# Kernel tuning notes

Hardware: AMD Instinct MI355X
Metric: run time of the kernel (lower is better)

## Reference

```python
import jax, jax.numpy as jnp
import numpy as np

SEQ_LEN = 2048
EMB = 512
BATCH = 8


def _xavier_uniform(key, shape):
    fan_in, fan_out = shape[0], shape[1]
    bound = float(np.sqrt(6.0 / (fan_in + fan_out)))
    return jax.random.uniform(key, shape, dtype=jnp.float32, minval=-bound, maxval=bound)


def setup_inputs() -> dict:
    key = jax.random.key(0)
    kx, k1, k2 = jax.random.split(key, 3)
    x = jax.random.normal(kx, (BATCH, EMB, SEQ_LEN), dtype=jnp.float32)
    weight1 = _xavier_uniform(k1, (EMB, EMB))
    weight2 = _xavier_uniform(k2, (EMB, EMB))
    return {"x": x, "weight1": weight1, "weight2": weight2}


def reference(x, weight1, weight2):
    # x: [b, e, s]
    s = x.shape[-1]
    # projections: O(b*s*e^2)
    fitnesses1 = jnp.einsum('bes,ef->bfs', x, weight1)   # [b, e, s]
    fitnesses2 = jnp.einsum('bfs,ef->bes', x, weight2)   # [b, e, s]
    # s x t interaction matrix: O(b*s^2*e)
    weight = jnp.einsum('bes,bet->bst', fitnesses1, fitnesses2)  # [b, s, t]
    # zero strictly-upper triangle (t > s), as in torch.triu(..., diagonal=1)
    mask = jnp.triu(jnp.ones((s, s), dtype=bool), k=1)
    weight = jnp.where(mask, jnp.zeros((), dtype=weight.dtype), weight)
    fitnesses = jnp.einsum('bst,bet->bes', weight, x)    # [b, e, s]
    avg_fitness = jnp.einsum('bes,bes->be', x, fitnesses)[..., None]  # [b, e, 1]
    net_fitnesses = fitnesses - avg_fitness
    x_next = x + x * net_fitnesses
    return jax.nn.relu(x_next)
```

## Files before the change

### kernel.cpp

```cpp
#include <hip/hip_runtime.h>
#include <hip/hip_bf16.h>
#include <stdint.h>


#define SEQ 2048
#define EMB 512
#define NBATCH 8

typedef unsigned short u16;
typedef __bf16 bf16x8 __attribute__((ext_vector_type(8)));
typedef float f32x4 __attribute__((ext_vector_type(4)));
typedef u16 u16x8 __attribute__((ext_vector_type(8)));

#define AS1 __attribute__((address_space(1)))
#define AS3 __attribute__((address_space(3)))

#define SBAR do { __builtin_amdgcn_sched_barrier(0); __builtin_amdgcn_s_barrier(); \
                  __builtin_amdgcn_sched_barrier(0); } while (0)
#define LGKM0 do { asm volatile("s_waitcnt lgkmcnt(0)" ::: "memory"); \
                   __builtin_amdgcn_sched_barrier(0); } while (0)

__device__ __forceinline__ u16 f2bf(float f) {
  uint32_t u = __builtin_bit_cast(uint32_t, f);
  uint32_t r = u + 0x7FFFu + ((u >> 16) & 1u);
  return (u16)(r >> 16);
}
__device__ __forceinline__ float bf2f(u16 u) {
  return __builtin_bit_cast(float, (uint32_t)u << 16);
}
__device__ __forceinline__ void gld_lds16(const void* g, void* l) {
  __builtin_amdgcn_global_load_lds((AS1 uint32_t*)g, (AS3 uint32_t*)l, 16, 0, 0);
}

__global__ __launch_bounds__(256) void prep_x_kernel(const float* __restrict__ x,
    u16* __restrict__ xb, u16* __restrict__ xbT) {
  __shared__ float tile[64][65];
  const int b = blockIdx.z;
  const int s0 = blockIdx.x * 64, e0 = blockIdx.y * 64;
  const float* xin = x + (size_t)b * EMB * SEQ;
  const int tid = threadIdx.x;
  #pragma unroll
  for (int it = 0; it < 4; ++it) {
    int idx = it * 256 + tid;
    int r = idx >> 4, c4 = idx & 15;
    float4 v = *(const float4*)(xin + (size_t)(e0 + r) * SEQ + s0 + c4 * 4);
    tile[r][c4 * 4 + 0] = v.x; tile[r][c4 * 4 + 1] = v.y;
    tile[r][c4 * 4 + 2] = v.z; tile[r][c4 * 4 + 3] = v.w;
  }
  __syncthreads();
  u16* ob = xb + (size_t)b * EMB * SEQ;
  #pragma unroll
  for (int it = 0; it < 2; ++it) {
    int idx = it * 256 + tid; int r = idx >> 3, c8 = idx & 7;
    u16x8 o;
    #pragma unroll
    for (int q = 0; q < 8; ++q) o[q] = f2bf(tile[r][c8 * 8 + q]);
    *(u16x8*)(ob + (size_t)(e0 + r) * SEQ + s0 + c8 * 8) = o;
  }
  u16* obT = xbT + (size_t)b * SEQ * EMB;
  #pragma unroll
  for (int it = 0; it < 2; ++it) {
    int idx = it * 256 + tid; int r = idx >> 3, c8 = idx & 7;
    u16x8 o;
    #pragma unroll
    for (int q = 0; q < 8; ++q) o[q] = f2bf(tile[c8 * 8 + q][r]);
    *(u16x8*)(obT + (size_t)(s0 + r) * EMB + e0 + c8 * 8) = o;
  }
}

__global__ __launch_bounds__(256) void cast_bf16_kernel(const float* __restrict__ in,
                                                        u16* __restrict__ out, int n4) {
  int i = blockIdx.x * 256 + threadIdx.x;
  if (i >= n4) return;
  float4 v = reinterpret_cast<const float4*>(in)[i];
  ushort4 r;
  r.x = f2bf(v.x); r.y = f2bf(v.y); r.z = f2bf(v.z); r.w = f2bf(v.w);
  reinterpret_cast<ushort4*>(out)[i] = r;
}

__global__ __launch_bounds__(256) void transpose_cast_kernel(const float* __restrict__ in,
    u16* __restrict__ out, int R, int C) {
  __shared__ float tile[32][33];
  const int c0 = blockIdx.x * 32, r0 = blockIdx.y * 32;
  const int tx = threadIdx.x, ty = threadIdx.y;
  #pragma unroll
  for (int i = 0; i < 32; i += 8)
    tile[ty + i][tx] = in[(size_t)(r0 + ty + i) * C + c0 + tx];
  __syncthreads();
  #pragma unroll
  for (int i = 0; i < 32; i += 8)
    out[(size_t)(c0 + ty + i) * R + r0 + tx] = f2bf(tile[tx][ty + i]);
}

struct Smem {
  __align__(16) u16 LA[2][256 * 64];
  __align__(16) u16 LB[2][256 * 64];
};

__device__ __forceinline__ void gemm_pipe(const u16* __restrict__ Ab, int ldA,
    const u16* __restrict__ Bb, int ldB, int nk, Smem& sm, f32x4 (&acc)[8][4]) {
  const int tid  = threadIdx.x;
  const int lane = tid & 63;
  const int wave = tid >> 6;
  const int wr = wave >> 2;
  const int wc = wave & 3;

  auto stage_half = [&](const u16* gbase, int ldG, int rowOff, int kcol, u16* lds) {
    #pragma unroll
    for (int p = 0; p < 2; ++p) {
      int c = p * 512 + tid;
      int row = c >> 3, cc = c & 7;
      int cs = cc ^ (row & 7);
      gld_lds16(gbase + (size_t)(rowOff + row) * ldG + kcol + cs * 8,
                lds + (size_t)(p * 512 + wave * 64) * 8);
    }
  };
  auto ldfrag = [&](const u16* base, int rloc, int c2) -> bf16x8 {
    int cs = c2 ^ (rloc & 7);
    return *reinterpret_cast<const bf16x8*>(base + (size_t)(rloc * 8 + cs) * 8);
  };

  stage_half(Ab, ldA, 0,   0, sm.LA[0]);
  stage_half(Ab, ldA, 128, 0, sm.LA[0] + 8192);
  stage_half(Bb, ldB, 0,   0, sm.LB[0]);
  stage_half(Bb, ldB, 128, 0, sm.LB[0] + 8192);
  if (nk > 1) {
    stage_half(Bb, ldB, 0,   64, sm.LB[1]);
    stage_half(Bb, ldB, 128, 64, sm.LB[1] + 8192);
  }
  if (nk > 1) { asm volatile("s_waitcnt vmcnt(4)" ::: "memory"); }
  else        { asm volatile("s_waitcnt vmcnt(0)" ::: "memory"); }
  SBAR;

  const int ar = lane & 15;
  const int asel = lane >> 4;
  bf16x8 af[4][2], bf0[2][2], bf1[2][2];

  for (int t = 0; t < nk; ++t) {
    const int sel = t & 1;
    const u16* a_ = sm.LA[sel];
    const u16* b_ = sm.LB[sel];

    #pragma unroll
    for (int m = 0; m < 4; ++m)
      #pragma unroll
      for (int kk = 0; kk < 2; ++kk)
        af[m][kk] = ldfrag(a_, wr * 128 + m * 16 + ar, kk * 4 + asel);
    #pragma unroll
    for (int n = 0; n < 2; ++n)
      #pragma unroll
      for (int kk = 0; kk < 2; ++kk)
        bf0[n][kk] = ldfrag(b_, wc * 64 + n * 16 + ar, kk * 4 + asel);
    if (t + 1 < nk) stage_half(Ab, ldA, 0, (t + 1) * 64, sm.LA[sel ^ 1]);
    SBAR; LGKM0;
    __builtin_amdgcn_s_setprio(1);
    #pragma unroll
    for (int m = 0; m < 4; ++m)
      #pragma unroll
      for (int n = 0; n < 2; ++n)
        #pragma unroll
        for (int kk = 0; kk < 2; ++kk)
          acc[m][n] = __builtin_amdgcn_mfma_f32_16x16x32_bf16(af[m][kk], bf0[n][kk], acc[m][n], 0, 0, 0);
    __builtin_amdgcn_s_setprio(0);
    SBAR;

    #pragma unroll
    for (int n = 0; n < 2; ++n)
      #pragma unroll
      for (int kk = 0; kk < 2; ++kk)
        bf1[n][kk] = ldfrag(b_, wc * 64 + (n + 2) * 16 + ar, kk * 4 + asel);
    if (t + 1 < nk) stage_half(Ab, ldA, 128, (t + 1) * 64, sm.LA[sel ^ 1] + 8192);
    SBAR; LGKM0;
    __builtin_amdgcn_s_setprio(1);
    #pragma unroll
    for (int m = 0; m < 4; ++m)
      #pragma unroll
      for (int n = 0; n < 2; ++n)
        #pragma unroll
        for (int kk = 0; kk < 2; ++kk)
          acc[m][n + 2] = __builtin_amdgcn_mfma_f32_16x16x32_bf16(af[m][kk], bf1[n][kk], acc[m][n + 2], 0, 0, 0);
    __builtin_amdgcn_s_setprio(0);
    SBAR;

    #pragma unroll
    for (int m = 0; m < 4; ++m)
      #pragma unroll
      for (int kk = 0; kk < 2; ++kk)
        af[m][kk] = ldfrag(a_, wr * 128 + 64 + m * 16 + ar, kk * 4 + asel);
    if (t + 2 < nk) stage_half(Bb, ldB, 0, (t + 2) * 64, sm.LB[sel]);
    SBAR; LGKM0;
    __builtin_amdgcn_s_setprio(1);
    #pragma unroll
    for (int m = 0; m < 4; ++m)
      #pragma unroll
      for (int n = 0; n < 2; ++n)
        #pragma unroll
        for (int kk = 0; kk < 2; ++kk)
          acc[m + 4][n + 2] = __builtin_amdgcn_mfma_f32_16x16x32_bf16(af[m][kk], bf1[n][kk], acc[m + 4][n + 2], 0, 0, 0);
    __builtin_amdgcn_s_setprio(0);
    SBAR;

    if (t + 2 < nk) stage_half(Bb, ldB, 128, (t + 2) * 64, sm.LB[sel] + 8192);
    SBAR;
    __builtin_amdgcn_s_setprio(1);
    #pragma unroll
    for (int m = 0; m < 4; ++m)
      #pragma unroll
      for (int n = 0; n < 2; ++n)
        #pragma unroll
        for (int kk = 0; kk < 2; ++kk)
          acc[m + 4][n] = __builtin_amdgcn_mfma_f32_16x16x32_bf16(af[m][kk], bf0[n][kk], acc[m + 4][n], 0, 0, 0);
    __builtin_amdgcn_s_setprio(0);
    if (t + 1 < nk) {
      if (t + 2 < nk) { asm volatile("s_waitcnt vmcnt(4)" ::: "memory"); }
      else            { asm volatile("s_waitcnt vmcnt(0)" ::: "memory"); }
    }
    SBAR;
  }
}

template<int MODE>
__global__ __launch_bounds__(512, 2) void k_gemm(
    const u16* __restrict__ X1, const u16* __restrict__ X2,
    const u16* __restrict__ X3, const u16* __restrict__ X4,
    u16* __restrict__ O16, u16* __restrict__ O16b, float* __restrict__ O32) {
  __shared__ Smem sm;
  const int tid  = threadIdx.x;
  const int lane = tid & 63;
  const int wave = tid >> 6;
  const int wr = wave >> 2;
  const int wc = wave & 3;
  const int bz = blockIdx.z;

  f32x4 acc[8][4];
  #pragma unroll
  for (int i = 0; i < 8; ++i)
    #pragma unroll
    for (int j = 0; j < 4; ++j) acc[i][j] = (f32x4){0.f, 0.f, 0.f, 0.f};

  const int r0 = (lane >> 4) * 4;
  const int cn = lane & 15;

  if (MODE == 0) {
    const int bm = blockIdx.x, bn = blockIdx.y;
    const u16* A = X1 + (size_t)bz * SEQ * EMB + (size_t)(bm * 256) * 512;
    const u16* B = X2 + (size_t)(bn * 256) * 512;
    gemm_pipe(A, 512, B, 512, 8, sm, acc);
    u16* C = O16 + (size_t)bz * SEQ * 1024;
    #pragma unroll
    for (int m = 0; m < 8; ++m)
      #pragma unroll
      for (int n = 0; n < 4; ++n)
        #pragma unroll
        for (int r = 0; r < 4; ++r) {
          int lr = wr * 128 + m * 16 + r0 + r, lc = wc * 64 + n * 16 + cn;
          C[(size_t)(bm * 256 + lr) * 1024 + bn * 256 + lc] = f2bf(acc[m][n][r]);
        }
  } else if (MODE == 1) {
    const int xx = blockIdx.x;
    if (xx < 16) {
      const int m2 = xx >> 3, n2 = xx & 7;
      const u16* A = X1 + (size_t)(m2 * 256) * 512;
      const u16* B = X2 + (size_t)bz * SEQ * EMB + (size_t)(n2 * 256) * 512;
      gemm_pipe(A, 512, B, 512, 8, sm, acc);
      u16* C = O16 + (size_t)bz * EMB * SEQ;
      #pragma unroll
      for (int m = 0; m < 8; ++m)
        #pragma unroll
        for (int n = 0; n < 4; ++n)
          #pragma unroll
          for (int r = 0; r < 4; ++r) {
            int lr = wr * 128 + m * 16 + r0 + r, lc = wc * 64 + n * 16 + cn;
            C[(size_t)(m2 * 256 + lr) * SEQ + n2 * 256 + lc] = f2bf(acc[m][n][r]);
          }
    } else {
      const int i = xx - 16;
      const u16* Fb = X3 + (size_t)bz * SEQ * 1024;
      const u16* A = Fb + (size_t)(i * 256) * 1024;
      const u16* B = Fb + 512 + (size_t)(i * 256) * 1024;
      gemm_pipe(A, 1024, B, 1024, 8, sm, acc);
      u16* C = O16b + (size_t)(bz * 8 + i) * 256 * 256;
      #pragma unroll
      for (int m = 0; m < 8; ++m)
        #pragma unroll
        for (int n = 0; n < 4; ++n)
          #pragma unroll
          for (int r = 0; r < 4; ++r) {
            int lr = wr * 128 + m * 16 + r0 + r, lc = wc * 64 + n * 16 + cn;
            float v = (lc > lr) ? 0.f : acc[m][n][r];
            C[(size_t)lr * 256 + lc] = f2bf(v);
          }
    }
  } else if (MODE == 2) {
    const int m = blockIdx.x >> 1, n = blockIdx.x & 1;
    const int b = bz >> 3, j = bz & 7;
    const u16* A = X1 + (size_t)b * EMB * SEQ + (size_t)(m * 256) * SEQ + j * 256;
    const u16* B = X2 + (size_t)b * EMB * SEQ + (size_t)(n * 256) * SEQ + j * 256;
    gemm_pipe(A, SEQ, B, SEQ, 4, sm, acc);
    u16* C = O16 + (size_t)(b * 8 + j) * EMB * EMB;
    #pragma unroll
    for (int mm = 0; mm < 8; ++mm)
      #pragma unroll
      for (int nn = 0; nn < 4; ++nn)
        #pragma unroll
        for (int r = 0; r < 4; ++r) {
          int lr = wr * 128 + mm * 16 + r0 + r, lc = wc * 64 + nn * 16 + cn;
          C[(size_t)(m * 256 + lr) * EMB + n * 256 + lc] = f2bf(acc[mm][nn][r]);
        }
  } else {
    const int m = blockIdx.x & 1, i = blockIdx.x >> 1;
    if (i > 0) {
      const u16* A = X1 + (size_t)(bz * 7 + i - 1) * EMB * EMB + (size_t)(m * 256) * 512;
      const u16* B = X2 + (size_t)bz * SEQ * 1024 + (size_t)(i * 256) * 1024;
      gemm_pipe(A, 512, B, 1024, 8, sm, acc);
    }
    {
      const u16* A = X3 + (size_t)bz * EMB * SEQ + (size_t)(m * 256) * SEQ + i * 256;
      const u16* B = X4 + (size_t)(bz * 8 + i) * 256 * 256;
      gemm_pipe(A, SEQ, B, 256, 4, sm, acc);
    }
    float* C = O32 + (size_t)bz * EMB * SEQ;
    #pragma unroll
    for (int mm = 0; mm < 8; ++mm)
      #pragma unroll
      for (int nn = 0; nn < 4; ++nn)
        #pragma unroll
        for (int r = 0; r < 4; ++r) {
          int lr = wr * 128 + mm * 16 + r0 + r, lc = wc * 64 + nn * 16 + cn;
          C[(size_t)(m * 256 + lr) * SEQ + i * 256 + lc] = acc[mm][nn][r];
        }
  }
}

__global__ __launch_bounds__(256) void k_prefix(const u16* __restrict__ Gc,
                                                u16* __restrict__ Gp) {
  const int b = blockIdx.z;
  const size_t base = ((size_t)blockIdx.x * 256 + threadIdx.x) * 8;
  float run[8] = {0.f, 0.f, 0.f, 0.f, 0.f, 0.f, 0.f, 0.f};
  #pragma unroll
  for (int j = 0; j < 7; ++j) {
    u16x8 v = *(const u16x8*)(Gc + (size_t)(b * 8 + j) * EMB * EMB + base);
    u16x8 o;
    #pragma unroll
    for (int q = 0; q < 8; ++q) { run[q] += bf2f(v[q]); o[q] = f2bf(run[q]); }
    *(u16x8*)(Gp + (size_t)(b * 7 + j) * EMB * EMB + base) = o;
  }
}

__global__ __launch_bounds__(256) void finalize_kernel(const u16* __restrict__ xb,
    const float* __restrict__ fit, float* __restrict__ out) {
  const size_t row = blockIdx.x;
  const u16* xr = xb + row * SEQ;
  const float* fr = fit + row * SEQ;
  float* orow = out + row * SEQ;
  const int tid = threadIdx.x;

  float xv[2][4]; float4 fv[2];
  float part = 0.f;
  #pragma unroll
  for (int i = 0; i < 2; ++i) {
    const int s0 = i * 1024 + tid * 4;
    ushort4 xu = *reinterpret_cast<const ushort4*>(xr + s0);
    xv[i][0] = bf2f(xu.x); xv[i][1] = bf2f(xu.y); xv[i][2] = bf2f(xu.z); xv[i][3] = bf2f(xu.w);
    fv[i] = reinterpret_cast<const float4*>(fr)[i * 256 + tid];
    part += xv[i][0] * fv[i].x + xv[i][1] * fv[i].y + xv[i][2] * fv[i].z + xv[i][3] * fv[i].w;
  }
  #pragma unroll
  for (int off = 1; off < 64; off <<= 1) part += __shfl_xor(part, off);
  __shared__ float wsum[4];
  const int wave = tid >> 6, lane = tid & 63;
  if (lane == 0) wsum[wave] = part;
  __syncthreads();
  const float avg = wsum[0] + wsum[1] + wsum[2] + wsum[3];

  #pragma unroll
  for (int i = 0; i < 2; ++i) {
    float4 o;
    o.x = xv[i][0] * (1.f + fv[i].x - avg); o.x = o.x > 0.f ? o.x : 0.f;
    o.y = xv[i][1] * (1.f + fv[i].y - avg); o.y = o.y > 0.f ? o.y : 0.f;
    o.z = xv[i][2] * (1.f + fv[i].z - avg); o.z = o.z > 0.f ? o.z : 0.f;
    o.w = xv[i][3] * (1.f + fv[i].w - avg); o.w = o.w > 0.f ? o.w : 0.f;
    reinterpret_cast<float4*>(orow)[i * 256 + tid] = o;
  }
}

extern "C" void kernel_launch(void* const* d_in, const int* in_sizes, int n_in,
                              void* d_out, int out_size, void* d_ws, size_t ws_size,
                              hipStream_t stream) {
  const float* x  = (const float*)d_in[0];
  const float* W1 = (const float*)d_in[1];
  const float* W2 = (const float*)d_in[2];
  float* out = (float*)d_out;

  char* ws = (char*)d_ws;
  const size_t nX = (size_t)NBATCH * EMB * SEQ;

  size_t off = 0;
  u16* xb   = (u16*)(ws + off); off += nX * 2;
  u16* Fcat = (u16*)(ws + off); off += (size_t)NBATCH * SEQ * 1024 * 2;
  const size_t offOverlay = off;
  u16* xbT  = (u16*)(ws + off); off += nX * 2;
  u16* Wcat = (u16*)(ws + off); off += (size_t)1024 * 512 * 2;
  u16* F2n  = (u16*)(ws + off); off += nX * 2;
  u16* Sd   = (u16*)(ws + off); off += (size_t)NBATCH * 8 * 256 * 256 * 2;
  u16* Gc   = (u16*)(ws + off); off += (size_t)NBATCH * 8 * EMB * EMB * 2;
  u16* Gp   = (u16*)(ws + off); off += (size_t)NBATCH * 7 * EMB * EMB * 2;
  float* fit = (float*)(ws + offOverlay);

  prep_x_kernel<<<dim3(SEQ / 64, EMB / 64, NBATCH), 256, 0, stream>>>(x, xb, xbT);
  transpose_cast_kernel<<<dim3(EMB / 32, EMB / 32), dim3(32, 8), 0, stream>>>(W1, Wcat, EMB, EMB);
  cast_bf16_kernel<<<EMB * EMB / 4 / 256, 256, 0, stream>>>(W2, Wcat + (size_t)512 * 512, EMB * EMB / 4);

  k_gemm<0><<<dim3(8, 4, NBATCH), 512, 0, stream>>>(
      xbT, Wcat, nullptr, nullptr, Fcat, nullptr, nullptr);

  k_gemm<1><<<dim3(24, 1, NBATCH), 512, 0, stream>>>(
      Wcat + (size_t)512 * 512, xbT, Fcat, nullptr, F2n, Sd, nullptr);

  k_gemm<2><<<dim3(4, 1, 64), 512, 0, stream>>>(
      xb, F2n, nullptr, nullptr, Gc, nullptr, nullptr);

  k_prefix<<<dim3(128, 1, NBATCH), 256, 0, stream>>>(Gc, Gp);

  k_gemm<3><<<dim3(16, 1, NBATCH), 512, 0, stream>>>(
      Gp, Fcat, xb, Sd, nullptr, nullptr, fit);

  finalize_kernel<<<NBATCH * EMB, 256, 0, stream>>>(xb, fit, out);
}
```

Baseline: 133.7 us.

## Shrink GEMM tiles to 128x128 with 256 threads and drop double-buffered pipeline

Replaces the 256x256, 8-wave, double-buffered GEMM pipeline with a simple single-buffered 128x128 tile on 4 waves, and quadruples the grid of every GEMM launch. More blocks fill the GPU better and allow three resident blocks per CU. The sub-blocks that are entirely above the diagonal in the masked S tile only write zeros instead of running a matmul. The cost is that global loads are no longer overlapped with MFMA work, there is less reuse per tile, and each K step adds a full wait and barrier.

Result: slower. 140.2 us (+4.8%).

```diff
diff --git a/kernel.cpp b/kernel.cpp
--- a/kernel.cpp
+++ b/kernel.cpp
@@ -92,27 +92,24 @@
     out[(size_t)(c0 + ty + i) * R + r0 + tx] = f2bf(tile[tx][ty + i]);
 }
 
-struct Smem {
-  __align__(16) u16 LA[2][256 * 64];
-  __align__(16) u16 LB[2][256 * 64];
+struct Smem128 {
+  __align__(16) u16 LA[128 * 64];
+  __align__(16) u16 LB[128 * 64];
 };
 
-__device__ __forceinline__ void gemm_pipe(const u16* __restrict__ Ab, int ldA,
-    const u16* __restrict__ Bb, int ldB, int nk, Smem& sm, f32x4 (&acc)[8][4]) {
-  const int tid  = threadIdx.x;
-  const int lane = tid & 63;
-  const int wave = tid >> 6;
-  const int wr = wave >> 2;
-  const int wc = wave & 3;
-
-  auto stage_half = [&](const u16* gbase, int ldG, int rowOff, int kcol, u16* lds) {
-    #pragma unroll
-    for (int p = 0; p < 2; ++p) {
-      int c = p * 512 + tid;
-      int row = c >> 3, cc = c & 7;
-      int cs = cc ^ (row & 7);
-      gld_lds16(gbase + (size_t)(rowOff + row) * ldG + kcol + cs * 8,
-                lds + (size_t)(p * 512 + wave * 64) * 8);
+__device__ __forceinline__ void gemm128(const u16* __restrict__ Ab, int ldA,
+    const u16* __restrict__ Bb, int ldB, int nk, Smem128& sm, f32x4 (&acc)[4][4]) {
+  const int tid = threadIdx.x, lane = tid & 63, wave = tid >> 6;
+  const int wr = wave >> 1, wc = wave & 1;
+  const int ar = lane & 15, asel = lane >> 4;
+
+  auto stage = [&](const u16* g, int ld, int kcol, u16* lds) {
+    #pragma unroll
+    for (int it = 0; it < 4; ++it) {
+      int L = it * 256 + tid;
+      int row = L >> 3, cc = L & 7, cs = cc ^ (row & 7);
+      gld_lds16(g + (size_t)row * ld + kcol + cs * 8,
+                lds + (size_t)(it * 256 + wave * 64) * 8);
     }
   };
   auto ldfrag = [&](const u16* base, int rloc, int c2) -> bf16x8 {
@@ -120,121 +117,52 @@
     return *reinterpret_cast<const bf16x8*>(base + (size_t)(rloc * 8 + cs) * 8);
   };
 
-  stage_half(Ab, ldA, 0,   0, sm.LA[0]);
-  stage_half(Ab, ldA, 128, 0, sm.LA[0] + 8192);
-  stage_half(Bb, ldB, 0,   0, sm.LB[0]);
-  stage_half(Bb, ldB, 128, 0, sm.LB[0] + 8192);
-  if (nk > 1) {
-    stage_half(Bb, ldB, 0,   64, sm.LB[1]);
-    stage_half(Bb, ldB, 128, 64, sm.LB[1] + 8192);
-  }
-  if (nk > 1) { asm volatile("s_waitcnt vmcnt(4)" ::: "memory"); }
-  else        { asm volatile("s_waitcnt vmcnt(0)" ::: "memory"); }
-  SBAR;
-
-  const int ar = lane & 15;
-  const int asel = lane >> 4;
-  bf16x8 af[4][2], bf0[2][2], bf1[2][2];
-
   for (int t = 0; t < nk; ++t) {
-    const int sel = t & 1;
-    const u16* a_ = sm.LA[sel];
-    const u16* b_ = sm.LB[sel];
-
+    stage(Ab, ldA, t * 64, sm.LA);
+    stage(Bb, ldB, t * 64, sm.LB);
+    asm volatile("s_waitcnt vmcnt(0)" ::: "memory");
+    SBAR;
+    bf16x8 af[4][2], bf[4][2];
     #pragma unroll
     for (int m = 0; m < 4; ++m)
       #pragma unroll
       for (int kk = 0; kk < 2; ++kk)
-        af[m][kk] = ldfrag(a_, wr * 128 + m * 16 + ar, kk * 4 + asel);
-    #pragma unroll
-    for (int n = 0; n < 2; ++n)
+        af[m][kk] = ldfrag(sm.LA, wr * 64 + m * 16 + ar, kk * 4 + asel);
+    #pragma unroll
+    for (int n = 0; n < 4; ++n)
       #pragma unroll
       for (int kk = 0; kk < 2; ++kk)
-        bf0[n][kk] = ldfrag(b_, wc * 64 + n * 16 + ar, kk * 4 + asel);
-    if (t + 1 < nk) stage_half(Ab, ldA, 0, (t + 1) * 64, sm.LA[sel ^ 1]);
-    SBAR; LGKM0;
+        bf[n][kk] = ldfrag(sm.LB, wc * 64 + n * 16 + ar, kk * 4 + asel);
+    LGKM0;
     __builtin_amdgcn_s_setprio(1);
     #pragma unroll
     for (int m = 0; m < 4; ++m)
       #pragma unroll
-      for (int n = 0; n < 2; ++n)
+      for (int n = 0; n < 4; ++n)
         #pragma unroll
         for (int kk = 0; kk < 2; ++kk)
-          acc[m][n] = __builtin_amdgcn_mfma_f32_16x16x32_bf16(af[m][kk], bf0[n][kk], acc[m][n], 0, 0, 0);
+          acc[m][n] = __builtin_amdgcn_mfma_f32_16x16x32_bf16(af[m][kk], bf[n][kk], acc[m][n], 0, 0, 0);
     __builtin_amdgcn_s_setprio(0);
     SBAR;
-
-    #pragma unroll
-    for (int n = 0; n < 2; ++n)
-      #pragma unroll
-      for (int kk = 0; kk < 2; ++kk)
-        bf1[n][kk] = ldfrag(b_, wc * 64 + (n + 2) * 16 + ar, kk * 4 + asel);
-    if (t + 1 < nk) stage_half(Ab, ldA, 128, (t + 1) * 64, sm.LA[sel ^ 1] + 8192);
-    SBAR; LGKM0;
-    __builtin_amdgcn_s_setprio(1);
-    #pragma unroll
-    for (int m = 0; m < 4; ++m)
-      #pragma unroll
-      for (int n = 0; n < 2; ++n)
-        #pragma unroll
-        for (int kk = 0; kk < 2; ++kk)
-          acc[m][n + 2] = __builtin_amdgcn_mfma_f32_16x16x32_bf16(af[m][kk], bf1[n][kk], acc[m][n + 2], 0, 0, 0);
-    __builtin_amdgcn_s_setprio(0);
-    SBAR;
-
-    #pragma unroll
-    for (int m = 0; m < 4; ++m)
-      #pragma unroll
-      for (int kk = 0; kk < 2; ++kk)
-        af[m][kk] = ldfrag(a_, wr * 128 + 64 + m * 16 + ar, kk * 4 + asel);
-    if (t + 2 < nk) stage_half(Bb, ldB, 0, (t + 2) * 64, sm.LB[sel]);
-    SBAR; LGKM0;
-    __builtin_amdgcn_s_setprio(1);
-    #pragma unroll
-    for (int m = 0; m < 4; ++m)
-      #pragma unroll
-      for (int n = 0; n < 2; ++n)
-        #pragma unroll
-        for (int kk = 0; kk < 2; ++kk)
-          acc[m + 4][n + 2] = __builtin_amdgcn_mfma_f32_16x16x32_bf16(af[m][kk], bf1[n][kk], acc[m + 4][n + 2], 0, 0, 0);
-    __builtin_amdgcn_s_setprio(0);
-    SBAR;
-
-    if (t + 2 < nk) stage_half(Bb, ldB, 128, (t + 2) * 64, sm.LB[sel] + 8192);
-    SBAR;
-    __builtin_amdgcn_s_setprio(1);
-    #pragma unroll
-    for (int m = 0; m < 4; ++m)
-      #pragma unroll
-      for (int n = 0; n < 2; ++n)
-        #pragma unroll
-        for (int kk = 0; kk < 2; ++kk)
-          acc[m + 4][n] = __builtin_amdgcn_mfma_f32_16x16x32_bf16(af[m][kk], bf0[n][kk], acc[m + 4][n], 0, 0, 0);
-    __builtin_amdgcn_s_setprio(0);
-    if (t + 1 < nk) {
-      if (t + 2 < nk) { asm volatile("s_waitcnt vmcnt(4)" ::: "memory"); }
-      else            { asm volatile("s_waitcnt vmcnt(0)" ::: "memory"); }
-    }
-    SBAR;
   }
 }
 
 template<int MODE>
-__global__ __launch_bounds__(512, 2) void k_gemm(
+__global__ __launch_bounds__(256, 3) void k_gemm(
     const u16* __restrict__ X1, const u16* __restrict__ X2,
     const u16* __restrict__ X3, const u16* __restrict__ X4,
     u16* __restrict__ O16, u16* __restrict__ O16b, float* __restrict__ O32) {
-  __shared__ Smem sm;
+  __shared__ Smem128 sm;
   const int tid  = threadIdx.x;
   const int lane = tid & 63;
   const int wave = tid >> 6;
-  const int wr = wave >> 2;
-  const int wc = wave & 3;
+  const int wr = wave >> 1;
+  const int wc = wave & 1;
   const int bz = blockIdx.z;
 
-  f32x4 acc[8][4];
-  #pragma unroll
-  for (int i = 0; i < 8; ++i)
+  f32x4 acc[4][4];
+  #pragma unroll
+  for (int i = 0; i < 4; ++i)
     #pragma unroll
     for (int j = 0; j < 4; ++j) acc[i][j] = (f32x4){0.f, 0.f, 0.f, 0.f};
 
@@ -242,92 +170,104 @@
   const int cn = lane & 15;
 
   if (MODE == 0) {
-    const int bm = blockIdx.x, bn = blockIdx.y;
-    const u16* A = X1 + (size_t)bz * SEQ * EMB + (size_t)(bm * 256) * 512;
-    const u16* B = X2 + (size_t)(bn * 256) * 512;
-    gemm_pipe(A, 512, B, 512, 8, sm, acc);
+    const int m = blockIdx.x, n = blockIdx.y;
+    const u16* A = X1 + (size_t)bz * SEQ * EMB + (size_t)(m * 128) * 512;
+    const u16* B = X2 + (size_t)(n * 128) * 512;
+    gemm128(A, 512, B, 512, 8, sm, acc);
     u16* C = O16 + (size_t)bz * SEQ * 1024;
     #pragma unroll
-    for (int m = 0; m < 8; ++m)
-      #pragma unroll
-      for (int n = 0; n < 4; ++n)
+    for (int mm = 0; mm < 4; ++mm)
+      #pragma unroll
+      for (int nn = 0; nn < 4; ++nn)
         #pragma unroll
         for (int r = 0; r < 4; ++r) {
-          int lr = wr * 128 + m * 16 + r0 + r, lc = wc * 64 + n * 16 + cn;
-          C[(size_t)(bm * 256 + lr) * 1024 + bn * 256 + lc] = f2bf(acc[m][n][r]);
+          int lr = wr * 64 + mm * 16 + r0 + r, lc = wc * 64 + nn * 16 + cn;
+          C[(size_t)(m * 128 + lr) * 1024 + n * 128 + lc] = f2bf(acc[mm][nn][r]);
         }
   } else if (MODE == 1) {
     const int xx = blockIdx.x;
-    if (xx < 16) {
-      const int m2 = xx >> 3, n2 = xx & 7;
-      const u16* A = X1 + (size_t)(m2 * 256) * 512;
-      const u16* B = X2 + (size_t)bz * SEQ * EMB + (size_t)(n2 * 256) * 512;
-      gemm_pipe(A, 512, B, 512, 8, sm, acc);
+    if (xx < 64) {
+      const int m2 = xx >> 4, n2 = xx & 15;
+      const u16* A = X1 + (size_t)(m2 * 128) * 512;
+      const u16* B = X2 + (size_t)bz * SEQ * EMB + (size_t)(n2 * 128) * 512;
+      gemm128(A, 512, B, 512, 8, sm, acc);
       u16* C = O16 + (size_t)bz * EMB * SEQ;
       #pragma unroll
-      for (int m = 0; m < 8; ++m)
-        #pragma unroll
-        for (int n = 0; n < 4; ++n)
+      for (int mm = 0; mm < 4; ++mm)
+        #pragma unroll
+        for (int nn = 0; nn < 4; ++nn)
           #pragma unroll
           for (int r = 0; r < 4; ++r) {
-            int lr = wr * 128 + m * 16 + r0 + r, lc = wc * 64 + n * 16 + cn;
-            C[(size_t)(m2 * 256 + lr) * SEQ + n2 * 256 + lc] = f2bf(acc[m][n][r]);
+            int lr = wr * 64 + mm * 16 + r0 + r, lc = wc * 64 + nn * 16 + cn;
+            C[(size_t)(m2 * 128 + lr) * SEQ + n2 * 128 + lc] = f2bf(acc[mm][nn][r]);
           }
     } else {
-      const int i = xx - 16;
+      const int idx = xx - 64;
+      const int i = idx >> 2, p = (idx >> 1) & 1, q = idx & 1;
+      u16* C = O16b + (size_t)(bz * 8 + i) * 256 * 256;
+      if (p == 0 && q == 1) {
+        u16x8 z = {0, 0, 0, 0, 0, 0, 0, 0};
+        #pragma unroll
+        for (int it = 0; it < 8; ++it) {
+          int id2 = it * 256 + tid;
+          int r = id2 >> 4, c8 = id2 & 15;
+          *(u16x8*)(C + (size_t)r * 256 + 128 + c8 * 8) = z;
+        }
+        return;
+      }
       const u16* Fb = X3 + (size_t)bz * SEQ * 1024;
-      const u16* A = Fb + (size_t)(i * 256) * 1024;
-      const u16* B = Fb + 512 + (size_t)(i * 256) * 1024;
-      gemm_pipe(A, 1024, B, 1024, 8, sm, acc);
-      u16* C = O16b + (size_t)(bz * 8 + i) * 256 * 256;
-      #pragma unroll
-      for (int m = 0; m < 8; ++m)
-        #pragma unroll
-        for (int n = 0; n < 4; ++n)
+      const u16* A = Fb + (size_t)(i * 256 + p * 128) * 1024;
+      const u16* B = Fb + 512 + (size_t)(i * 256 + q * 128) * 1024;
+      gemm128(A, 1024, B, 1024, 8, sm, acc);
+      #pragma unroll
+      for (int mm = 0; mm < 4; ++mm)
+        #pragma unroll
+        for (int nn = 0; nn < 4; ++nn)
           #pragma unroll
           for (int r = 0; r < 4; ++r) {
-            int lr = wr * 128 + m * 16 + r0 + r, lc = wc * 64 + n * 16 + cn;
-            float v = (lc > lr) ? 0.f : acc[m][n][r];
-            C[(size_t)lr * 256 + lc] = f2bf(v);
+            int lr = wr * 64 + mm * 16 + r0 + r, lc = wc * 64 + nn * 16 + cn;
+            int grow = p * 128 + lr, gcol = q * 128 + lc;
+            float v = (gcol > grow) ? 0.f : acc[mm][nn][r];
+            C[(size_t)grow * 256 + gcol] = f2bf(v);
           }
     }
   } else if (MODE == 2) {
-    const int m = blockIdx.x >> 1, n = blockIdx.x & 1;
+    const int m = blockIdx.x >> 2, n = blockIdx.x & 3;
     const int b = bz >> 3, j = bz & 7;
-    const u16* A = X1 + (size_t)b * EMB * SEQ + (size_t)(m * 256) * SEQ + j * 256;
-    const u16* B = X2 + (size_t)b * EMB * SEQ + (size_t)(n * 256) * SEQ + j * 256;
-    gemm_pipe(A, SEQ, B, SEQ, 4, sm, acc);
+    const u16* A = X1 + (size_t)b * EMB * SEQ + (size_t)(m * 128) * SEQ + j * 256;
+    const u16* B = X2 + (size_t)b * EMB * SEQ + (size_t)(n * 128) * SEQ + j * 256;
+    gemm128(A, SEQ, B, SEQ, 4, sm, acc);
     u16* C = O16 + (size_t)(b * 8 + j) * EMB * EMB;
     #pragma unroll
-    for (int mm = 0; mm < 8; ++mm)
+    for (int mm = 0; mm < 4; ++mm)
       #pragma unroll
       for (int nn = 0; nn < 4; ++nn)
         #pragma unroll
         for (int r = 0; r < 4; ++r) {
-          int lr = wr * 128 + mm * 16 + r0 + r, lc = wc * 64 + nn * 16 + cn;
-          C[(size_t)(m * 256 + lr) * EMB + n * 256 + lc] = f2bf(acc[mm][nn][r]);
+          int lr = wr * 64 + mm * 16 + r0 + r, lc = wc * 64 + nn * 16 + cn;
+          C[(size_t)(m * 128 + lr) * EMB + n * 128 + lc] = f2bf(acc[mm][nn][r]);
         }
   } else {
-    const int m = blockIdx.x & 1, i = blockIdx.x >> 1;
+    const int m = blockIdx.x >> 1, n = blockIdx.x & 1, i = blockIdx.y;
     if (i > 0) {
-      const u16* A = X1 + (size_t)(bz * 7 + i - 1) * EMB * EMB + (size_t)(m * 256) * 512;
-      const u16* B = X2 + (size_t)bz * SEQ * 1024 + (size_t)(i * 256) * 1024;
-      gemm_pipe(A, 512, B, 1024, 8, sm, acc);
+      const u16* A = X1 + (size_t)(bz * 7 + i - 1) * EMB * EMB + (size_t)(m * 128) * 512;
+      const u16* B = X2 + (size_t)bz * SEQ * 1024 + (size_t)(i * 256 + n * 128) * 1024;
+      gemm128(A, 512, B, 1024, 8, sm, acc);
     }
     {
-      const u16* A = X3 + (size_t)bz * EMB * SEQ + (size_t)(m * 256) * SEQ + i * 256;
-      const u16* B = X4 + (size_t)(bz * 8 + i) * 256 * 256;
-      gemm_pipe(A, SEQ, B, 256, 4, sm, acc);
+      const u16* A = X3 + (size_t)bz * EMB * SEQ + (size_t)(m * 128) * SEQ + i * 256;
+      const u16* B = X4 + (size_t)(bz * 8 + i) * 256 * 256 + (size_t)(n * 128) * 256;
+      gemm128(A, SEQ, B, 256, 4, sm, acc);
     }
     float* C = O32 + (size_t)bz * EMB * SEQ;
     #pragma unroll
-    for (int mm = 0; mm < 8; ++mm)
+    for (int mm = 0; mm < 4; ++mm)
       #pragma unroll
       for (int nn = 0; nn < 4; ++nn)
         #pragma unroll
         for (int r = 0; r < 4; ++r) {
-          int lr = wr * 128 + mm * 16 + r0 + r, lc = wc * 64 + nn * 16 + cn;
-          C[(size_t)(m * 256 + lr) * SEQ + i * 256 + lc] = acc[mm][nn][r];
+          int lr = wr * 64 + mm * 16 + r0 + r, lc = wc * 64 + nn * 16 + cn;
+          C[(size_t)(m * 128 + lr) * SEQ + i * 256 + n * 128 + lc] = acc[mm][nn][r];
         }
   }
 }
@@ -411,18 +351,18 @@
   transpose_cast_kernel<<<dim3(EMB / 32, EMB / 32), dim3(32, 8), 0, stream>>>(W1, Wcat, EMB, EMB);
   cast_bf16_kernel<<<EMB * EMB / 4 / 256, 256, 0, stream>>>(W2, Wcat + (size_t)512 * 512, EMB * EMB / 4);
 
-  k_gemm<0><<<dim3(8, 4, NBATCH), 512, 0, stream>>>(
+  k_gemm<0><<<dim3(16, 8, NBATCH), 256, 0, stream>>>(
       xbT, Wcat, nullptr, nullptr, Fcat, nullptr, nullptr);
 
-  k_gemm<1><<<dim3(24, 1, NBATCH), 512, 0, stream>>>(
+  k_gemm<1><<<dim3(96, 1, NBATCH), 256, 0, stream>>>(
       Wcat + (size_t)512 * 512, xbT, Fcat, nullptr, F2n, Sd, nullptr);
 
-  k_gemm<2><<<dim3(4, 1, 64), 512, 0, stream>>>(
+  k_gemm<2><<<dim3(16, 1, 64), 256, 0, stream>>>(
       xb, F2n, nullptr, nullptr, Gc, nullptr, nullptr);
 
   k_prefix<<<dim3(128, 1, NBATCH), 256, 0, stream>>>(Gc, Gp);
 
-  k_gemm<3><<<dim3(16, 1, NBATCH), 512, 0, stream>>>(
+  k_gemm<3><<<dim3(8, 8, NBATCH), 256, 0, stream>>>(
       Gp, Fcat, xb, Sd, nullptr, nullptr, fit);
 
   finalize_kernel<<<NBATCH * EMB, 256, 0, stream>>>(xb, fit, out);
```

## Merge GEMM launches, fuse weight prep, and chain fitness GEMM phases in one pipeline

Applied to the files above, without the earlier changes.

Merges the two weight-prep kernels into one launch, and moves the F2 projection into the first GEMM launch alongside F1. The Sd diagonal-block GEMM and the per-chunk Gram GEMM now share one launch, so the pipeline has fewer kernel launches and less idle tail per launch. The final GEMM streams both phases (prefix-Gram times F1, then x times masked diagonal) through a single continuous pipeline through a parameter lambda, so there is no pipeline drain between them. It also stores the fitness result in bf16 instead of fp32, which halves that round trip but adds rounding error before the avg reduction.

Result: no change. 135.4 us (+1.3%).

```diff
diff --git a/kernel.cpp b/kernel.cpp
--- a/kernel.cpp
+++ b/kernel.cpp
@@ -68,28 +68,26 @@
   }
 }
 
-__global__ __launch_bounds__(256) void cast_bf16_kernel(const float* __restrict__ in,
-                                                        u16* __restrict__ out, int n4) {
-  int i = blockIdx.x * 256 + threadIdx.x;
-  if (i >= n4) return;
-  float4 v = reinterpret_cast<const float4*>(in)[i];
-  ushort4 r;
-  r.x = f2bf(v.x); r.y = f2bf(v.y); r.z = f2bf(v.z); r.w = f2bf(v.w);
-  reinterpret_cast<ushort4*>(out)[i] = r;
-}
-
-__global__ __launch_bounds__(256) void transpose_cast_kernel(const float* __restrict__ in,
-    u16* __restrict__ out, int R, int C) {
+__global__ __launch_bounds__(256) void prep_w_kernel(const float* __restrict__ W1,
+    const float* __restrict__ W2, u16* __restrict__ Wcat) {
   __shared__ float tile[32][33];
   const int c0 = blockIdx.x * 32, r0 = blockIdx.y * 32;
   const int tx = threadIdx.x, ty = threadIdx.y;
-  #pragma unroll
-  for (int i = 0; i < 32; i += 8)
-    tile[ty + i][tx] = in[(size_t)(r0 + ty + i) * C + c0 + tx];
-  __syncthreads();
-  #pragma unroll
-  for (int i = 0; i < 32; i += 8)
-    out[(size_t)(c0 + ty + i) * R + r0 + tx] = f2bf(tile[tx][ty + i]);
+  if (blockIdx.z == 0) {
+    #pragma unroll
+    for (int i = 0; i < 32; i += 8)
+      tile[ty + i][tx] = W1[(size_t)(r0 + ty + i) * EMB + c0 + tx];
+    __syncthreads();
+    #pragma unroll
+    for (int i = 0; i < 32; i += 8)
+      Wcat[(size_t)(c0 + ty + i) * EMB + r0 + tx] = f2bf(tile[tx][ty + i]);
+  } else {
+    u16* W2b = Wcat + (size_t)512 * 512;
+    #pragma unroll
+    for (int i = 0; i < 32; i += 8)
+      W2b[(size_t)(r0 + ty + i) * EMB + c0 + tx] =
+          f2bf(W2[(size_t)(r0 + ty + i) * EMB + c0 + tx]);
+  }
 }
 
 struct Smem {
@@ -97,21 +95,23 @@
   __align__(16) u16 LB[2][256 * 64];
 };
 
-__device__ __forceinline__ void gemm_pipe(const u16* __restrict__ Ab, int ldA,
-    const u16* __restrict__ Bb, int ldB, int nk, Smem& sm, f32x4 (&acc)[8][4]) {
+template<typename PAR>
+__device__ __forceinline__ void gemm_pipe(PAR par, int nk, Smem& sm, f32x4 (&acc)[8][4]) {
   const int tid  = threadIdx.x;
   const int lane = tid & 63;
   const int wave = tid >> 6;
   const int wr = wave >> 2;
   const int wc = wave & 3;
 
-  auto stage_half = [&](const u16* gbase, int ldG, int rowOff, int kcol, u16* lds) {
+  auto stage_half = [&](int t, int ab, int half, u16* lds) {
+    const u16* g; int ld, k;
+    par(t, ab, g, ld, k);
     #pragma unroll
     for (int p = 0; p < 2; ++p) {
       int c = p * 512 + tid;
       int row = c >> 3, cc = c & 7;
       int cs = cc ^ (row & 7);
-      gld_lds16(gbase + (size_t)(rowOff + row) * ldG + kcol + cs * 8,
+      gld_lds16(g + (size_t)(half * 128 + row) * ld + k + cs * 8,
                 lds + (size_t)(p * 512 + wave * 64) * 8);
     }
   };
@@ -120,13 +120,13 @@
     return *reinterpret_cast<const bf16x8*>(base + (size_t)(rloc * 8 + cs) * 8);
   };
 
-  stage_half(Ab, ldA, 0,   0, sm.LA[0]);
-  stage_half(Ab, ldA, 128, 0, sm.LA[0] + 8192);
-  stage_half(Bb, ldB, 0,   0, sm.LB[0]);
-  stage_half(Bb, ldB, 128, 0, sm.LB[0] + 8192);
+  stage_half(0, 0, 0, sm.LA[0]);
+  stage_half(0, 0, 1, sm.LA[0] + 8192);
+  stage_half(0, 1, 0, sm.LB[0]);
+  stage_half(0, 1, 1, sm.LB[0] + 8192);
   if (nk > 1) {
-    stage_half(Bb, ldB, 0,   64, sm.LB[1]);
-    stage_half(Bb, ldB, 128, 64, sm.LB[1] + 8192);
+    stage_half(1, 1, 0, sm.LB[1]);
+    stage_half(1, 1, 1, sm.LB[1] + 8192);
   }
   if (nk > 1) { asm volatile("s_waitcnt vmcnt(4)" ::: "memory"); }
   else        { asm volatile("s_waitcnt vmcnt(0)" ::: "memory"); }
@@ -151,7 +151,7 @@
       #pragma unroll
       for (int kk = 0; kk < 2; ++kk)
         bf0[n][kk] = ldfrag(b_, wc * 64 + n * 16 + ar, kk * 4 + asel);
-    if (t + 1 < nk) stage_half(Ab, ldA, 0, (t + 1) * 64, sm.LA[sel ^ 1]);
+    if (t + 1 < nk) stage_half(t + 1, 0, 0, sm.LA[sel ^ 1]);
     SBAR; LGKM0;
     __builtin_amdgcn_s_setprio(1);
     #pragma unroll
@@ -169,7 +169,7 @@
       #pragma unroll
       for (int kk = 0; kk < 2; ++kk)
         bf1[n][kk] = ldfrag(b_, wc * 64 + (n + 2) * 16 + ar, kk * 4 + asel);
-    if (t + 1 < nk) stage_half(Ab, ldA, 128, (t + 1) * 64, sm.LA[sel ^ 1] + 8192);
+    if (t + 1 < nk) stage_half(t + 1, 0, 1, sm.LA[sel ^ 1] + 8192);
     SBAR; LGKM0;
     __builtin_amdgcn_s_setprio(1);
     #pragma unroll
@@ -187,7 +187,7 @@
       #pragma unroll
       for (int kk = 0; kk < 2; ++kk)
         af[m][kk] = ldfrag(a_, wr * 128 + 64 + m * 16 + ar, kk * 4 + asel);
-    if (t + 2 < nk) stage_half(Bb, ldB, 0, (t + 2) * 64, sm.LB[sel]);
+    if (t + 2 < nk) stage_half(t + 2, 1, 0, sm.LB[sel]);
     SBAR; LGKM0;
     __builtin_amdgcn_s_setprio(1);
     #pragma unroll
@@ -200,7 +200,7 @@
     __builtin_amdgcn_s_setprio(0);
     SBAR;
 
-    if (t + 2 < nk) stage_half(Bb, ldB, 128, (t + 2) * 64, sm.LB[sel] + 8192);
+    if (t + 2 < nk) stage_half(t + 2, 1, 1, sm.LB[sel] + 8192);
     SBAR;
     __builtin_amdgcn_s_setprio(1);
     #pragma unroll
@@ -223,7 +223,7 @@
 __global__ __launch_bounds__(512, 2) void k_gemm(
     const u16* __restrict__ X1, const u16* __restrict__ X2,
     const u16* __restrict__ X3, const u16* __restrict__ X4,
-    u16* __restrict__ O16, u16* __restrict__ O16b, float* __restrict__ O32) {
+    u16* __restrict__ O16, u16* __restrict__ O16b) {
   __shared__ Smem sm;
   const int tid  = threadIdx.x;
   const int lane = tid & 63;
@@ -242,62 +242,107 @@
   const int cn = lane & 15;
 
   if (MODE == 0) {
-    const int bm = blockIdx.x, bn = blockIdx.y;
-    const u16* A = X1 + (size_t)bz * SEQ * EMB + (size_t)(bm * 256) * 512;
-    const u16* B = X2 + (size_t)(bn * 256) * 512;
-    gemm_pipe(A, 512, B, 512, 8, sm, acc);
-    u16* C = O16 + (size_t)bz * SEQ * 1024;
-    #pragma unroll
-    for (int m = 0; m < 8; ++m)
-      #pragma unroll
-      for (int n = 0; n < 4; ++n)
-        #pragma unroll
-        for (int r = 0; r < 4; ++r) {
-          int lr = wr * 128 + m * 16 + r0 + r, lc = wc * 64 + n * 16 + cn;
-          C[(size_t)(bm * 256 + lr) * 1024 + bn * 256 + lc] = f2bf(acc[m][n][r]);
-        }
+    const int xx = blockIdx.x;
+    const u16* Ap; const u16* Bp;
+    if (xx < 32) {
+      const int m = xx >> 2, n = xx & 3;
+      Ap = X1 + (size_t)bz * SEQ * EMB + (size_t)(m * 256) * 512;
+      Bp = X2 + (size_t)(n * 256) * 512;
+      auto par = [&](int t, int ab, const u16*& g, int& ld, int& k) {
+        g = ab ? Bp : Ap; ld = 512; k = t * 64;
+      };
+      gemm_pipe(par, 8, sm, acc);
+      u16* C = O16 + (size_t)bz * SEQ * 1024;
+      #pragma unroll
+      for (int mm = 0; mm < 8; ++mm)
+        #pragma unroll
+        for (int nn = 0; nn < 4; ++nn)
+          #pragma unroll
+          for (int r = 0; r < 4; ++r) {
+            int lr = wr * 128 + mm * 16 + r0 + r, lc = wc * 64 + nn * 16 + cn;
+            C[(size_t)(m * 256 + lr) * 1024 + n * 256 + lc] = f2bf(acc[mm][nn][r]);
+          }
+    } else {
+      const int m2 = (xx - 32) >> 3, n2 = (xx - 32) & 7;
+      Ap = X2 + (size_t)512 * 512 + (size_t)(m2 * 256) * 512;
+      Bp = X1 + (size_t)bz * SEQ * EMB + (size_t)(n2 * 256) * 512;
+      auto par = [&](int t, int ab, const u16*& g, int& ld, int& k) {
+        g = ab ? Bp : Ap; ld = 512; k = t * 64;
+      };
+      gemm_pipe(par, 8, sm, acc);
+      u16* C = O16b + (size_t)bz * EMB * SEQ;
+      #pragma unroll
+      for (int mm = 0; mm < 8; ++mm)
+        #pragma unroll
+        for (int nn = 0; nn < 4; ++nn)
+          #pragma unroll
+          for (int r = 0; r < 4; ++r) {
+            int lr = wr * 128 + mm * 16 + r0 + r, lc = wc * 64 + nn * 16 + cn;
+            C[(size_t)(m2 * 256 + lr) * SEQ + n2 * 256 + lc] = f2bf(acc[mm][nn][r]);
+          }
+    }
   } else if (MODE == 1) {
     const int xx = blockIdx.x;
-    if (xx < 16) {
-      const int m2 = xx >> 3, n2 = xx & 7;
-      const u16* A = X1 + (size_t)(m2 * 256) * 512;
-      const u16* B = X2 + (size_t)bz * SEQ * EMB + (size_t)(n2 * 256) * 512;
-      gemm_pipe(A, 512, B, 512, 8, sm, acc);
-      u16* C = O16 + (size_t)bz * EMB * SEQ;
-      #pragma unroll
-      for (int m = 0; m < 8; ++m)
-        #pragma unroll
-        for (int n = 0; n < 4; ++n)
+    if (xx < 8) {
+      const int i = xx;
+      const u16* Fb = X1 + (size_t)bz * SEQ * 1024;
+      const u16* Ap = Fb + (size_t)(i * 256) * 1024;
+      const u16* Bp = Fb + 512 + (size_t)(i * 256) * 1024;
+      auto par = [&](int t, int ab, const u16*& g, int& ld, int& k) {
+        g = ab ? Bp : Ap; ld = 1024; k = t * 64;
+      };
+      gemm_pipe(par, 8, sm, acc);
+      u16* C = O16 + (size_t)(bz * 8 + i) * 256 * 256;
+      #pragma unroll
+      for (int mm = 0; mm < 8; ++mm)
+        #pragma unroll
+        for (int nn = 0; nn < 4; ++nn)
           #pragma unroll
           for (int r = 0; r < 4; ++r) {
-            int lr = wr * 128 + m * 16 + r0 + r, lc = wc * 64 + n * 16 + cn;
-            C[(size_t)(m2 * 256 + lr) * SEQ + n2 * 256 + lc] = f2bf(acc[m][n][r]);
+            int lr = wr * 128 + mm * 16 + r0 + r, lc = wc * 64 + nn * 16 + cn;
+            float v = (lc > lr) ? 0.f : acc[mm][nn][r];
+            C[(size_t)lr * 256 + lc] = f2bf(v);
           }
     } else {
-      const int i = xx - 16;
-      const u16* Fb = X3 + (size_t)bz * SEQ * 1024;
-      const u16* A = Fb + (size_t)(i * 256) * 1024;
-      const u16* B = Fb + 512 + (size_t)(i * 256) * 1024;
-      gemm_pipe(A, 1024, B, 1024, 8, sm, acc);
-      u16* C = O16b + (size_t)(bz * 8 + i) * 256 * 256;
-      #pragma unroll
-      for (int m = 0; m < 8; ++m)
-        #pragma unroll
-        for (int n = 0; n < 4; ++n)
+      const int y = xx - 8;
+      const int j = y >> 2, m = (y >> 1) & 1, n = y & 1;
+      const u16* Ap = X2 + (size_t)bz * EMB * SEQ + (size_t)(m * 256) * SEQ + j * 256;
+      const u16* Bp = X3 + (size_t)bz * EMB * SEQ + (size_t)(n * 256) * SEQ + j * 256;
+      auto par = [&](int t, int ab, const u16*& g, int& ld, int& k) {
+        g = ab ? Bp : Ap; ld = SEQ; k = t * 64;
+      };
+      gemm_pipe(par, 4, sm, acc);
+      u16* C = O16b + (size_t)(bz * 8 + j) * EMB * EMB;
+      #pragma unroll
+      for (int mm = 0; mm < 8; ++mm)
+        #pragma unroll
+        for (int nn = 0; nn < 4; ++nn)
           #pragma unroll
           for (int r = 0; r < 4; ++r) {
-            int lr = wr * 128 + m * 16 + r0 + r, lc = wc * 64 + n * 16 + cn;
-            float v = (lc > lr) ? 0.f : acc[m][n][r];
-            C[(size_t)lr * 256 + lc] = f2bf(v);
+            int lr = wr * 128 + mm * 16 + r0 + r, lc = wc * 64 + nn * 16 + cn;
+            C[(size_t)(m * 256 + lr) * EMB + n * 256 + lc] = f2bf(acc[mm][nn][r]);
           }
     }
-  } else if (MODE == 2) {
-    const int m = blockIdx.x >> 1, n = blockIdx.x & 1;
-    const int b = bz >> 3, j = bz & 7;
-    const u16* A = X1 + (size_t)b * EMB * SEQ + (size_t)(m * 256) * SEQ + j * 256;
-    const u16* B = X2 + (size_t)b * EMB * SEQ + (size_t)(n * 256) * SEQ + j * 256;
-    gemm_pipe(A, SEQ, B, SEQ, 4, sm, acc);
-    u16* C = O16 + (size_t)(b * 8 + j) * EMB * EMB;
+  } else {
+    const int i = blockIdx.x >> 1, m = blockIdx.x & 1;
+    const u16* Agp = (i > 0) ? X1 + (size_t)(bz * 7 + i - 1) * EMB * EMB + (size_t)(m * 256) * 512
+                             : X1;
+    const u16* Bf1 = X2 + (size_t)bz * SEQ * 1024 + (size_t)(i * 256) * 1024;
+    const u16* Axb = X3 + (size_t)bz * EMB * SEQ + (size_t)(m * 256) * SEQ;
+    const u16* Bsd = X4 + (size_t)(bz * 8 + i) * 256 * 256;
+    auto par = [&](int t, int ab, const u16*& g, int& ld, int& k) {
+      int tt = (i > 0) ? t : t + 8;
+      if (tt < 8) {
+        if (!ab) { g = Agp; ld = 512;  k = tt * 64; }
+        else     { g = Bf1; ld = 1024; k = tt * 64; }
+      } else {
+        int u = tt - 8;
+        if (!ab) { g = Axb; ld = SEQ; k = i * 256 + u * 64; }
+        else     { g = Bsd; ld = 256; k = u * 64; }
+      }
+    };
+    gemm_pipe(par, (i > 0) ? 12 : 4, sm, acc);
+    u16* C = O16 + (size_t)bz * EMB * SEQ;
     #pragma unroll
     for (int mm = 0; mm < 8; ++mm)
       #pragma unroll
@@ -305,29 +350,7 @@
         #pragma unroll
         for (int r = 0; r < 4; ++r) {
           int lr = wr * 128 + mm * 16 + r0 + r, lc = wc * 64 + nn * 16 + cn;
-          C[(size_t)(m * 256 + lr) * EMB + n * 256 + lc] = f2bf(acc[mm][nn][r]);
-        }
-  } else {
-    const int m = blockIdx.x & 1, i = blockIdx.x >> 1;
-    if (i > 0) {
-      const u16* A = X1 + (size_t)(bz * 7 + i - 1) * EMB * EMB + (size_t)(m * 256) * 512;
-      const u16* B = X2 + (size_t)bz * SEQ * 1024 + (size_t)(i * 256) * 1024;
-      gemm_pipe(A, 512, B, 1024, 8, sm, acc);
-    }
-    {
-      const u16* A = X3 + (size_t)bz * EMB * SEQ + (size_t)(m * 256) * SEQ + i * 256;
-      const u16* B = X4 + (size_t)(bz * 8 + i) * 256 * 256;
-      gemm_pipe(A, SEQ, B, 256, 4, sm, acc);
-    }
-    float* C = O32 + (size_t)bz * EMB * SEQ;
-    #pragma unroll
-    for (int mm = 0; mm < 8; ++mm)
-      #pragma unroll
-      for (int nn = 0; nn < 4; ++nn)
-        #pragma unroll
-        for (int r = 0; r < 4; ++r) {
-          int lr = wr * 128 + mm * 16 + r0 + r, lc = wc * 64 + nn * 16 + cn;
-          C[(size_t)(m * 256 + lr) * SEQ + i * 256 + lc] = acc[mm][nn][r];
+          C[(size_t)(m * 256 + lr) * SEQ + i * 256 + lc] = f2bf(acc[mm][nn][r]);
         }
   }
 }
@@ -348,22 +371,23 @@
 }
 
 __global__ __launch_bounds__(256) void finalize_kernel(const u16* __restrict__ xb,
-    const float* __restrict__ fit, float* __restrict__ out) {
+    const u16* __restrict__ fitb, float* __restrict__ out) {
   const size_t row = blockIdx.x;
   const u16* xr = xb + row * SEQ;
-  const float* fr = fit + row * SEQ;
+  const u16* fr = fitb + row * SEQ;
   float* orow = out + row * SEQ;
   const int tid = threadIdx.x;
 
-  float xv[2][4]; float4 fv[2];
+  float xv[2][4], fv[2][4];
   float part = 0.f;
   #pragma unroll
   for (int i = 0; i < 2; ++i) {
     const int s0 = i * 1024 + tid * 4;
     ushort4 xu = *reinterpret_cast<const ushort4*>(xr + s0);
+    ushort4 fu = *reinterpret_cast<const ushort4*>(fr + s0);
     xv[i][0] = bf2f(xu.x); xv[i][1] = bf2f(xu.y); xv[i][2] = bf2f(xu.z); xv[i][3] = bf2f(xu.w);
-    fv[i] = reinterpret_cast<const float4*>(fr)[i * 256 + tid];
-    part += xv[i][0] * fv[i].x + xv[i][1] * fv[i].y + xv[i][2] * fv[i].z + xv[i][3] * fv[i].w;
+    fv[i][0] = bf2f(fu.x); fv[i][1] = bf2f(fu.y); fv[i][2] = bf2f(fu.z); fv[i][3] = bf2f(fu.w);
+    part += xv[i][0] * fv[i][0] + xv[i][1] * fv[i][1] + xv[i][2] * fv[i][2] + xv[i][3] * fv[i][3];
   }
   #pragma unroll
   for (int off = 1; off < 64; off <<= 1) part += __shfl_xor(part, off);
@@ -376,10 +400,10 @@
   #pragma unroll
   for (int i = 0; i < 2; ++i) {
     float4 o;
-    o.x = xv[i][0] * (1.f + fv[i].x - avg); o.x = o.x > 0.f ? o.x : 0.f;
-    o.y = xv[i][1] * (1.f + fv[i].y - avg); o.y = o.y > 0.f ? o.y : 0.f;
-    o.z = xv[i][2] * (1.f + fv[i].z - avg); o.z = o.z > 0.f ? o.z : 0.f;
-    o.w = xv[i][3] * (1.f + fv[i].w - avg); o.w = o.w > 0.f ? o.w : 0.f;
+    o.x = xv[i][0] * (1.f + fv[i][0] - avg); o.x = o.x > 0.f ? o.x : 0.f;
+    o.y = xv[i][1] * (1.f + fv[i][1] - avg); o.y = o.y > 0.f ? o.y : 0.f;
+    o.z = xv[i][2] * (1.f + fv[i][2] - avg); o.z = o.z > 0.f ? o.z : 0.f;
+    o.w = xv[i][3] * (1.f + fv[i][3] - avg); o.w = o.w > 0.f ? o.w : 0.f;
     reinterpret_cast<float4*>(orow)[i * 256 + tid] = o;
   }
 }
@@ -405,25 +429,21 @@
   u16* Sd   = (u16*)(ws + off); off += (size_t)NBATCH * 8 * 256 * 256 * 2;
   u16* Gc   = (u16*)(ws + off); off += (size_t)NBATCH * 8 * EMB * EMB * 2;
   u16* Gp   = (u16*)(ws + off); off += (size_t)NBATCH * 7 * EMB * EMB * 2;
-  float* fit = (float*)(ws + offOverlay);
+  u16* fitb = (u16*)(ws + offOverlay);
 
   prep_x_kernel<<<dim3(SEQ / 64, EMB / 64, NBATCH), 256, 0, stream>>>(x, xb, xbT);
-  transpose_cast_kernel<<<dim3(EMB / 32, EMB / 32), dim3(32, 8), 0, stream>>>(W1, Wcat, EMB, EMB);
-  cast_bf16_kernel<<<EMB * EMB / 4 / 256, 256, 0, stream>>>(W2, Wcat + (size_t)512 * 512, EMB * EMB / 4);
-
-  k_gemm<0><<<dim3(8, 4, NBATCH), 512, 0, stream>>>(
-      xbT, Wcat, nullptr, nullptr, Fcat, nullptr, nullptr);
-
-  k_gemm<1><<<dim3(24, 1, NBATCH), 512, 0, stream>>>(
-      Wcat + (size_t)512 * 512, xbT, Fcat, nullptr, F2n, Sd, nullptr);
-
-  k_gemm<2><<<dim3(4, 1, 64), 512, 0, stream>>>(
-      xb, F2n, nullptr, nullptr, Gc, nullptr, nullptr);
+  prep_w_kernel<<<dim3(16, 16, 2), dim3(32, 8), 0, stream>>>(W1, W2, Wcat);
+
+  k_gemm<0><<<dim3(48, 1, NBATCH), 512, 0, stream>>>(
+      xbT, Wcat, nullptr, nullptr, Fcat, F2n);
+
+  k_gemm<1><<<dim3(40, 1, NBATCH), 512, 0, stream>>>(
+      Fcat, xb, F2n, nullptr, Sd, Gc);
 
   k_prefix<<<dim3(128, 1, NBATCH), 256, 0, stream>>>(Gc, Gp);
 
-  k_gemm<3><<<dim3(16, 1, NBATCH), 512, 0, stream>>>(
-      Gp, Fcat, xb, Sd, nullptr, nullptr, fit);
-
-  finalize_kernel<<<NBATCH * EMB, 256, 0, stream>>>(xb, fit, out);
-}
+  k_gemm<2><<<dim3(16, 1, NBATCH), 512, 0, stream>>>(
+      Gp, Fcat, xb, Sd, fitb, nullptr);
+
+  finalize_kernel<<<NBATCH * EMB, 256, 0, stream>>>(xb, fitb, out);
+}
```
